# Kernel tuning notes

Hardware: AMD Instinct MI355X
Metric: run time of the kernel (lower is better)

Reference implementation:

```python
import jax, jax.numpy as jnp
import numpy as np

N_NODES = 50000
NEG_SLOPE = 0.2  # PyG GATConv default
EPS = 1e-16      # PyG softmax eps


def gat_conv(x, src, dst, W, a_s, a_d, b, n_nodes):
    """One PyG-style GATConv layer (concat heads). a_s/a_d: [H, C]."""
    H, C = a_s.shape
    h = (x @ W).reshape(n_nodes, H, C)                   # [N, H, C]
    al_s = jnp.sum(h * a_s[None], axis=-1)               # [N, H]
    al_d = jnp.sum(h * a_d[None], axis=-1)               # [N, H]
    e = jax.nn.leaky_relu(al_s[src] + al_d[dst], NEG_SLOPE)  # [E, H]
    # segment softmax over incoming edges of each destination node
    m = jax.ops.segment_max(e, dst, num_segments=n_nodes)
    m = jnp.where(jnp.isfinite(m), m, 0.0)
    ex = jnp.exp(e - m[dst])
    denom = jax.ops.segment_sum(ex, dst, num_segments=n_nodes)
    alpha = ex / (denom[dst] + EPS)                       # [E, H]
    out = jax.ops.segment_sum(alpha[:, :, None] * h[src], dst, num_segments=n_nodes)
    return out.reshape(n_nodes, H * C) + b                # concat heads + bias


def setup_inputs() -> dict:
    key = jax.random.key(0)
    ks = jax.random.split(key, 16)
    s = 0.05
    return {
        "x": jax.random.normal(ks[0], (N_NODES, 256), jnp.float32),
        "edge_index": jax.random.randint(ks[1], (2, 800000), 0, N_NODES, jnp.int64),
        "W1": jax.random.normal(ks[2], (256, 256), jnp.float32) * s,
        "as1": jax.random.normal(ks[3], (4, 64), jnp.float32) * s,
        "ad1": jax.random.normal(ks[4], (4, 64), jnp.float32) * s,
        "b1": jnp.zeros((256,), jnp.float32),
        "W2": jax.random.normal(ks[5], (256, 256), jnp.float32) * s,
        "as2": jax.random.normal(ks[6], (4, 64), jnp.float32) * s,
        "ad2": jax.random.normal(ks[7], (4, 64), jnp.float32) * s,
        "b2": jnp.zeros((256,), jnp.float32),
        "W3": jax.random.normal(ks[8], (256, 128), jnp.float32) * s,
        "as3": jax.random.normal(ks[9], (1, 128), jnp.float32) * s,
        "ad3": jax.random.normal(ks[10], (1, 128), jnp.float32) * s,
        "b3": jnp.zeros((128,), jnp.float32),
    }


def reference(x, edge_index, W1, as1, ad1, b1, W2, as2, ad2, b2, W3, as3, ad3, b3):
    n = x.shape[0]
    loop = jnp.arange(n, dtype=edge_index.dtype)
    src = jnp.concatenate([edge_index[0], loop])  # add_self_loops=True (PyG default)
    dst = jnp.concatenate([edge_index[1], loop])
    # F.dropout(p=0.6, training=False) -> identity in eval
    h = gat_conv(x, src, dst, W1, as1, ad1, b1, n)
    h = jax.nn.elu(h)  # gnn_act='elu'
    h = gat_conv(h, src, dst, W2, as2, ad2, b2, n)
    h = jax.nn.elu(h)
    h = gat_conv(h, src, dst, W3, as3, ad3, b3, n)
    return h
```

## Files before the change

### kernel.cpp

```cpp
#include <hip/hip_runtime.h>
#include <math.h>


#define NEG_SLOPE 0.2f
#define EPS_SM 1e-16f

typedef _Float16 half8 __attribute__((ext_vector_type(8)));
typedef _Float16 half4v __attribute__((ext_vector_type(4)));
typedef _Float16 half2v __attribute__((ext_vector_type(2)));
typedef float f32x4 __attribute__((ext_vector_type(4)));

__device__ __forceinline__ float wave_allred_sum(float v) {
#pragma unroll
    for (int o = 32; o > 0; o >>= 1) v += __shfl_xor(v, o, 64);
    return v;
}
__device__ __forceinline__ float4 lrelu4(float4 v) {
    v.x = (v.x < 0.f) ? NEG_SLOPE * v.x : v.x;
    v.y = (v.y < 0.f) ? NEG_SLOPE * v.y : v.y;
    v.z = (v.z < 0.f) ? NEG_SLOPE * v.z : v.z;
    v.w = (v.w < 0.f) ? NEG_SLOPE * v.w : v.w;
    return v;
}

__global__ void hist_kernel(const int* __restrict__ ei, int E, int N,
                            int* __restrict__ cnt) {
    int e = blockIdx.x * 256 + threadIdx.x;
    int ET = E + N;
    if (e >= ET) return;
    int dst = (e < E) ? ei[E + e] : (e - E);
    atomicAdd(&cnt[dst], 1);
}

__global__ void scan_block(const int* __restrict__ cnt, int n_cnt,
                           int* __restrict__ offs, int n_off,
                           int* __restrict__ bsums) {
    __shared__ int buf[1024];
    int gid = blockIdx.x * 1024 + threadIdx.x;
    int v = (gid < n_cnt) ? cnt[gid] : 0;
    buf[threadIdx.x] = v;
    __syncthreads();
#pragma unroll
    for (int off = 1; off < 1024; off <<= 1) {
        int t = (threadIdx.x >= off) ? buf[threadIdx.x - off] : 0;
        __syncthreads();
        buf[threadIdx.x] += t;
        __syncthreads();
    }
    if (gid < n_off) offs[gid] = buf[threadIdx.x] - v;
    if (threadIdx.x == 1023) bsums[blockIdx.x] = buf[1023];
}

__global__ void scan_sums(int* __restrict__ bsums, int nb) {
    int l = threadIdx.x;
    int v = (l < nb) ? bsums[l] : 0;
    int s = v;
#pragma unroll
    for (int o = 1; o < 64; o <<= 1) {
        int t = __shfl_up(s, o, 64);
        if (l >= o) s += t;
    }
    if (l < nb) bsums[l] = s - v;
}

__global__ void scan_add(int* __restrict__ offs, int n_off,
                         const int* __restrict__ bsums) {
    int gid = blockIdx.x * 1024 + threadIdx.x;
    if (gid < n_off) offs[gid] += bsums[blockIdx.x];
}

__global__ void fill_csr(const int* __restrict__ ei, int E, int N,
                         const int* __restrict__ offs, int* __restrict__ fil,
                         int* __restrict__ csr) {
    int e = blockIdx.x * 256 + threadIdx.x;
    int ET = E + N;
    if (e >= ET) return;
    int src, dst;
    if (e < E) { src = ei[e]; dst = ei[E + e]; }
    else       { src = dst = e - E; }
    int pos = offs[dst] + atomicAdd(&fil[dst], 1);
    csr[pos] = src;
}

__global__ void wcast_all(const float* __restrict__ W1,
                          const float* __restrict__ W2,
                          const float* __restrict__ W3,
                          _Float16* __restrict__ o1,
                          _Float16* __restrict__ o2,
                          _Float16* __restrict__ o3) {
    int i = blockIdx.x * 256 + threadIdx.x;
    const float* W; _Float16* o; int K = 256, N, s;
    if (i < 65536)        { W = W1; o = o1; N = 256; s = i; }
    else if (i < 131072)  { W = W2; o = o2; N = 256; s = i - 65536; }
    else if (i < 163840)  { W = W3; o = o3; N = 128; s = i - 131072; }
    else return;
    int n = s / K, k = s - n * K;
    o[s] = (_Float16)W[(size_t)k * N + n];
}

template <bool AF32>
__global__ __launch_bounds__(256) void gemm_wide64(
    const void* __restrict__ Ain, const _Float16* __restrict__ Bt,
    _Float16* __restrict__ C,
    const float* __restrict__ a_s, const float* __restrict__ a_d,
    float* __restrict__ als, float* __restrict__ ald, int M) {
    const int K = 256, N = 256;
    __shared__ _Float16 As[2][64][40], Bs[2][256][40];
    const int bm = blockIdx.x * 64;
    const int tid = threadIdx.x;
    const int w = tid >> 6, lane = tid & 63;
    const int wn = w * 64;
    const int l16 = lane & 15, q = lane >> 4;
    const int kq = q * 8;
    const int arow = tid >> 2, ak = (tid & 3) * 8;
    const int brow = tid;
    const int agrow = bm + arow;
    const int NT = K >> 5;

    f32x4 acc[4][4];
#pragma unroll
    for (int i = 0; i < 4; ++i)
#pragma unroll
        for (int j = 0; j < 4; ++j) acc[i][j] = (f32x4){0.f, 0.f, 0.f, 0.f};

    half8 ra, rb0, rb1, rb2, rb3;
    auto LOAD = [&](int kt) {
        if constexpr (AF32) {
            const float* Af = (const float*)Ain;
            float4 v0, v1;
            if (agrow < M) {
                const float4* ap = (const float4*)(Af + (size_t)agrow * K + kt + ak);
                v0 = ap[0]; v1 = ap[1];
            } else {
                v0 = v1 = make_float4(0.f, 0.f, 0.f, 0.f);
            }
            ra[0] = (_Float16)v0.x; ra[1] = (_Float16)v0.y;
            ra[2] = (_Float16)v0.z; ra[3] = (_Float16)v0.w;
            ra[4] = (_Float16)v1.x; ra[5] = (_Float16)v1.y;
            ra[6] = (_Float16)v1.z; ra[7] = (_Float16)v1.w;
        } else {
            const _Float16* Ah = (const _Float16*)Ain;
            if (agrow < M) {
                ra = *(const half8*)(Ah + (size_t)agrow * K + kt + ak);
            } else {
                ra = (half8)(_Float16)0;
            }
        }
        const half8* bp = (const half8*)(Bt + (size_t)brow * K + kt);
        rb0 = bp[0]; rb1 = bp[1]; rb2 = bp[2]; rb3 = bp[3];
    };
    auto STORE = [&](int nb) {
        *(half8*)&As[nb][arow][ak]  = ra;
        *(half8*)&Bs[nb][brow][0]   = rb0;
        *(half8*)&Bs[nb][brow][8]   = rb1;
        *(half8*)&Bs[nb][brow][16]  = rb2;
        *(half8*)&Bs[nb][brow][24]  = rb3;
    };

    LOAD(0);
    STORE(0);
    int cur = 0;
    for (int kb = 0; kb < NT; ++kb) {
        const bool more = (kb + 1) < NT;
        if (more) LOAD((kb + 1) * 32);
        __syncthreads();
        half8 a[4], b[4];
#pragma unroll
        for (int t = 0; t < 4; ++t) {
            a[t] = *(const half8*)&As[cur][t * 16 + l16][kq];
            b[t] = *(const half8*)&Bs[cur][wn + t * 16 + l16][kq];
        }
#pragma unroll
        for (int i = 0; i < 4; ++i)
#pragma unroll
            for (int j = 0; j < 4; ++j)
                acc[i][j] = __builtin_amdgcn_mfma_f32_16x16x32_f16(
                    a[i], b[j], acc[i][j], 0, 0, 0);
        if (more) STORE(cur ^ 1);
        cur ^= 1;
    }

#pragma unroll
    for (int i = 0; i < 4; ++i) {
#pragma unroll
        for (int r = 0; r < 4; ++r) {
            int orow = bm + i * 16 + q * 4 + r;
            float c0 = acc[i][0][r], c1 = acc[i][1][r];
            float c2 = acc[i][2][r], c3 = acc[i][3][r];
            if (orow < M) {
                _Float16* cp = C + (size_t)orow * N + wn + l16;
                cp[0]  = (_Float16)c0;
                cp[16] = (_Float16)c1;
                cp[32] = (_Float16)c2;
                cp[48] = (_Float16)c3;
            }
            {
                const int cg = wn + l16;
                float ps = c0 * a_s[cg] + c1 * a_s[cg + 16] +
                           c2 * a_s[cg + 32] + c3 * a_s[cg + 48];
                float pd = c0 * a_d[cg] + c1 * a_d[cg + 16] +
                           c2 * a_d[cg + 32] + c3 * a_d[cg + 48];
#pragma unroll
                for (int o = 1; o < 16; o <<= 1) {
                    ps += __shfl_xor(ps, o, 64);
                    pd += __shfl_xor(pd, o, 64);
                }
                if (l16 == 0 && orow < M) {
                    als[orow * 4 + w] = ps;
                    ald[orow * 4 + w] = pd;
                }
            }
        }
    }
}

__global__ __launch_bounds__(256) void gemm_f16_l3(
    const _Float16* __restrict__ Ain, const _Float16* __restrict__ Bt,
    _Float16* __restrict__ C,
    const float* __restrict__ a_s, const float* __restrict__ a_d,
    float* __restrict__ als, float* __restrict__ ald,
    int M, int N, int K) {
    __shared__ _Float16 As[2][128][40], Bs[2][128][40];
    __shared__ float s_als[128], s_ald[128];
    const int bm = blockIdx.y * 128;
    const int tid = threadIdx.x;
    const int w = tid >> 6, lane = tid & 63;
    const int wm = (w >> 1) * 64, wn = (w & 1) * 64;
    const int l16 = lane & 15, q = lane >> 4;
    const int kq = q * 8;
    const int sr = tid >> 1;
    const int sk = (tid & 1) * 16;
    const int row = bm + sr;
    const int NT = K >> 5;

    f32x4 acc[4][4];
#pragma unroll
    for (int i = 0; i < 4; ++i)
#pragma unroll
        for (int j = 0; j < 4; ++j) acc[i][j] = (f32x4){0.f, 0.f, 0.f, 0.f};

    half8 ra0, ra1, rb0, rb1;
    auto LOAD = [&](int kt) {
        if (row < M) {
            const half8* ap = (const half8*)(Ain + (size_t)row * K + kt + sk);
            ra0 = ap[0]; ra1 = ap[1];
        } else {
            ra0 = (half8)(_Float16)0; ra1 = (half8)(_Float16)0;
        }
        const half8* bp = (const half8*)(Bt + (size_t)sr * K + kt + sk);
        rb0 = bp[0]; rb1 = bp[1];
    };
    auto STORE = [&](int nb) {
        *(half8*)&As[nb][sr][sk]     = ra0;
        *(half8*)&As[nb][sr][sk + 8] = ra1;
        *(half8*)&Bs[nb][sr][sk]     = rb0;
        *(half8*)&Bs[nb][sr][sk + 8] = rb1;
    };

    LOAD(0);
    STORE(0);
    int cur = 0;
    for (int kb = 0; kb < NT; ++kb) {
        const bool more = (kb + 1) < NT;
        if (more) LOAD((kb + 1) * 32);
        __syncthreads();
        half8 a[4], b[4];
#pragma unroll
        for (int t = 0; t < 4; ++t) {
            a[t] = *(const half8*)&As[cur][wm + t * 16 + l16][kq];
            b[t] = *(const half8*)&Bs[cur][wn + t * 16 + l16][kq];
        }
#pragma unroll
        for (int i = 0; i < 4; ++i)
#pragma unroll
            for (int j = 0; j < 4; ++j)
                acc[i][j] = __builtin_amdgcn_mfma_f32_16x16x32_f16(
                    a[i], b[j], acc[i][j], 0, 0, 0);
        if (more) STORE(cur ^ 1);
        cur ^= 1;
    }

    __syncthreads();
    if (tid < 128) { s_als[tid] = 0.f; s_ald[tid] = 0.f; }
    __syncthreads();
#pragma unroll
    for (int i = 0; i < 4; ++i) {
#pragma unroll
        for (int r = 0; r < 4; ++r) {
            int orow = bm + wm + i * 16 + q * 4 + r;
            float c0 = acc[i][0][r], c1 = acc[i][1][r];
            float c2 = acc[i][2][r], c3 = acc[i][3][r];
            if (orow < M) {
                _Float16* cp = C + (size_t)orow * N + wn + l16;
                cp[0]  = (_Float16)c0;
                cp[16] = (_Float16)c1;
                cp[32] = (_Float16)c2;
                cp[48] = (_Float16)c3;
            }
            {
                const int cg = wn + l16;
                float ps = c0 * a_s[cg] + c1 * a_s[cg + 16] +
                           c2 * a_s[cg + 32] + c3 * a_s[cg + 48];
                float pd = c0 * a_d[cg] + c1 * a_d[cg + 16] +
                           c2 * a_d[cg + 32] + c3 * a_d[cg + 48];
#pragma unroll
                for (int o = 1; o < 16; o <<= 1) {
                    ps += __shfl_xor(ps, o, 64);
                    pd += __shfl_xor(pd, o, 64);
                }
                if (l16 == 0) {
                    atomicAdd(&s_als[wm + i * 16 + q * 4 + r], ps);
                    atomicAdd(&s_ald[wm + i * 16 + q * 4 + r], pd);
                }
            }
        }
    }
    __syncthreads();
    if (tid < 128) {
        int orow = bm + tid;
        if (orow < M) { als[orow] = s_als[tid]; ald[orow] = s_ald[tid]; }
    }
}

template <bool ACT>
__global__ __launch_bounds__(256) void aggregate_h4_f16(
    const _Float16* __restrict__ h, const float4* __restrict__ als4,
    const float4* __restrict__ ald4, const int* __restrict__ offs,
    const int* __restrict__ csr, const float* __restrict__ bias,
    _Float16* __restrict__ out, int Nn) {
    const int tid = threadIdx.x;
    const int w = tid >> 6;
    const int l = tid & 63;
    const int n = blockIdx.x * 4 + w;
    __shared__ float s_alpha[4][64][4];
    __shared__ int s_src[4][64];
    if (n >= Nn) return;

    const int base = offs[n];
    const int deg = offs[n + 1] - base;
    const float4 adv = ald4[n];
    const int head = l >> 4;

    float4 acc = make_float4(0.f, 0.f, 0.f, 0.f);
    float4 den = make_float4(0.f, 0.f, 0.f, 0.f);
    for (int c0 = 0; c0 < deg; c0 += 64) {
        const int cl = min(64, deg - c0);
        if (l < cl) {
            int s = csr[base + c0 + l];
            float4 a = als4[s];
            float4 sc = lrelu4(make_float4(a.x + adv.x, a.y + adv.y,
                                           a.z + adv.z, a.w + adv.w));
            float4 ex = make_float4(__expf(sc.x), __expf(sc.y),
                                    __expf(sc.z), __expf(sc.w));
            *(float4*)&s_alpha[w][l][0] = ex;
            s_src[w][l] = s;
            den.x += ex.x; den.y += ex.y; den.z += ex.z; den.w += ex.w;
        }
        int e = 0;
        for (; e + 4 <= cl; e += 4) {
            int s0 = s_src[w][e + 0], s1 = s_src[w][e + 1];
            int s2 = s_src[w][e + 2], s3 = s_src[w][e + 3];
            float a0 = s_alpha[w][e + 0][head];
            float a1 = s_alpha[w][e + 1][head];
            float a2 = s_alpha[w][e + 2][head];
            float a3 = s_alpha[w][e + 3][head];
            half4v hv0 = *(const half4v*)(h + (size_t)s0 * 256 + l * 4);
            half4v hv1 = *(const half4v*)(h + (size_t)s1 * 256 + l * 4);
            half4v hv2 = *(const half4v*)(h + (size_t)s2 * 256 + l * 4);
            half4v hv3 = *(const half4v*)(h + (size_t)s3 * 256 + l * 4);
            acc.x = fmaf(a0, (float)hv0[0], acc.x);
            acc.y = fmaf(a0, (float)hv0[1], acc.y);
            acc.z = fmaf(a0, (float)hv0[2], acc.z);
            acc.w = fmaf(a0, (float)hv0[3], acc.w);
            acc.x = fmaf(a1, (float)hv1[0], acc.x);
            acc.y = fmaf(a1, (float)hv1[1], acc.y);
            acc.z = fmaf(a1, (float)hv1[2], acc.z);
            acc.w = fmaf(a1, (float)hv1[3], acc.w);
            acc.x = fmaf(a2, (float)hv2[0], acc.x);
            acc.y = fmaf(a2, (float)hv2[1], acc.y);
            acc.z = fmaf(a2, (float)hv2[2], acc.z);
            acc.w = fmaf(a2, (float)hv2[3], acc.w);
            acc.x = fmaf(a3, (float)hv3[0], acc.x);
            acc.y = fmaf(a3, (float)hv3[1], acc.y);
            acc.z = fmaf(a3, (float)hv3[2], acc.z);
            acc.w = fmaf(a3, (float)hv3[3], acc.w);
        }
        for (; e < cl; ++e) {
            int s0 = s_src[w][e];
            float a0 = s_alpha[w][e][head];
            half4v hv0 = *(const half4v*)(h + (size_t)s0 * 256 + l * 4);
            acc.x = fmaf(a0, (float)hv0[0], acc.x);
            acc.y = fmaf(a0, (float)hv0[1], acc.y);
            acc.z = fmaf(a0, (float)hv0[2], acc.z);
            acc.w = fmaf(a0, (float)hv0[3], acc.w);
        }
    }
    den.x = wave_allred_sum(den.x); den.y = wave_allred_sum(den.y);
    den.z = wave_allred_sum(den.z); den.w = wave_allred_sum(den.w);
    float d = (head == 0) ? den.x : (head == 1) ? den.y
             : (head == 2) ? den.z : den.w;
    const float rc = 1.f / (d + EPS_SM);

    float4 bv = *(const float4*)(bias + l * 4);
    float4 r = make_float4(acc.x * rc + bv.x, acc.y * rc + bv.y,
                           acc.z * rc + bv.z, acc.w * rc + bv.w);
    if (ACT) {
        r.x = (r.x > 0.f) ? r.x : expm1f(r.x);
        r.y = (r.y > 0.f) ? r.y : expm1f(r.y);
        r.z = (r.z > 0.f) ? r.z : expm1f(r.z);
        r.w = (r.w > 0.f) ? r.w : expm1f(r.w);
    }
    half4v ov = {(_Float16)r.x, (_Float16)r.y, (_Float16)r.z, (_Float16)r.w};
    *(half4v*)(out + (size_t)n * 256 + l * 4) = ov;
}

__global__ __launch_bounds__(256) void aggregate_h1_f16(
    const _Float16* __restrict__ h, const float* __restrict__ als,
    const float* __restrict__ ald, const int* __restrict__ offs,
    const int* __restrict__ csr, const float* __restrict__ bias,
    float* __restrict__ out, int Nn) {
    const int tid = threadIdx.x;
    const int w = tid >> 6;
    const int l = tid & 63;
    const int n = blockIdx.x * 4 + w;
    __shared__ float s_alpha[4][64];
    __shared__ int s_src[4][64];
    if (n >= Nn) return;

    const int base = offs[n];
    const int deg = offs[n + 1] - base;
    const float ad_n = ald[n];

    float2 acc = make_float2(0.f, 0.f);
    float den = 0.f;
    for (int c0 = 0; c0 < deg; c0 += 64) {
        const int cl = min(64, deg - c0);
        if (l < cl) {
            int s = csr[base + c0 + l];
            float sc = als[s] + ad_n;
            sc = (sc < 0.f) ? NEG_SLOPE * sc : sc;
            float ex = __expf(sc);
            s_alpha[w][l] = ex;
            s_src[w][l] = s;
            den += ex;
        }
        int e = 0;
        for (; e + 4 <= cl; e += 4) {
            int s0 = s_src[w][e + 0], s1 = s_src[w][e + 1];
            int s2 = s_src[w][e + 2], s3 = s_src[w][e + 3];
            float a0 = s_alpha[w][e + 0], a1 = s_alpha[w][e + 1];
            float a2 = s_alpha[w][e + 2], a3 = s_alpha[w][e + 3];
            half2v v0 = *(const half2v*)(h + (size_t)s0 * 128 + l * 2);
            half2v v1 = *(const half2v*)(h + (size_t)s1 * 128 + l * 2);
            half2v v2 = *(const half2v*)(h + (size_t)s2 * 128 + l * 2);
            half2v v3 = *(const half2v*)(h + (size_t)s3 * 128 + l * 2);
            acc.x = fmaf(a0, (float)v0[0], acc.x); acc.y = fmaf(a0, (float)v0[1], acc.y);
            acc.x = fmaf(a1, (float)v1[0], acc.x); acc.y = fmaf(a1, (float)v1[1], acc.y);
            acc.x = fmaf(a2, (float)v2[0], acc.x); acc.y = fmaf(a2, (float)v2[1], acc.y);
            acc.x = fmaf(a3, (float)v3[0], acc.x); acc.y = fmaf(a3, (float)v3[1], acc.y);
        }
        for (; e < cl; ++e) {
            int s0 = s_src[w][e];
            float a0 = s_alpha[w][e];
            half2v v0 = *(const half2v*)(h + (size_t)s0 * 128 + l * 2);
            acc.x = fmaf(a0, (float)v0[0], acc.x); acc.y = fmaf(a0, (float)v0[1], acc.y);
        }
    }
    den = wave_allred_sum(den);
    const float rc = 1.f / (den + EPS_SM);
    float2 r = make_float2(acc.x * rc + bias[l * 2],
                           acc.y * rc + bias[l * 2 + 1]);
    *(float2*)(out + (size_t)n * 128 + l * 2) = r;
}

extern "C" void kernel_launch(void* const* d_in, const int* in_sizes, int n_in,
                              void* d_out, int out_size, void* d_ws,
                              size_t ws_size, hipStream_t stream) {
    const float* x   = (const float*)d_in[0];
    const int*   ei  = (const int*)d_in[1];
    const float* W1  = (const float*)d_in[2];
    const float* as1 = (const float*)d_in[3];
    const float* ad1 = (const float*)d_in[4];
    const float* b1  = (const float*)d_in[5];
    const float* W2  = (const float*)d_in[6];
    const float* as2 = (const float*)d_in[7];
    const float* ad2 = (const float*)d_in[8];
    const float* b2  = (const float*)d_in[9];
    const float* W3  = (const float*)d_in[10];
    const float* as3 = (const float*)d_in[11];
    const float* ad3 = (const float*)d_in[12];
    const float* b3  = (const float*)d_in[13];

    const int Nn = in_sizes[0] / 256;
    const int E  = in_sizes[1] / 2;
    const int ET = E + Nn;

    char* p = (char*)d_ws;
    _Float16* bufA = (_Float16*)p; p += (size_t)Nn * 256 * 2;
    _Float16* bufB = (_Float16*)p; p += (size_t)Nn * 256 * 2;
    float* als  = (float*)p; p += (size_t)Nn * 4 * 4;
    float* ald  = (float*)p; p += (size_t)Nn * 4 * 4;
    int* cnt  = (int*)p; p += (size_t)Nn * 4;
    int* fil  = (int*)p; p += (size_t)Nn * 4;
    int* offs = (int*)p; p += (size_t)(Nn + 1) * 4;
    int* bsums = (int*)p; p += 256 * 4;
    int* csr  = (int*)p; p += (size_t)ET * 4;
    p = (char*)(((uintptr_t)p + 15) & ~(uintptr_t)15);
    _Float16* wt1 = (_Float16*)p; p += 256 * 256 * 2;
    _Float16* wt2 = (_Float16*)p; p += 256 * 256 * 2;
    _Float16* wt3 = (_Float16*)p; p += 128 * 256 * 2;

    hipMemsetAsync(cnt, 0, (size_t)2 * Nn * sizeof(int), stream);
    int nbE = (ET + 255) / 256;
    hist_kernel<<<nbE, 256, 0, stream>>>(ei, E, Nn, cnt);
    wcast_all<<<(163840 + 255) / 256, 256, 0, stream>>>(W1, W2, W3, wt1, wt2, wt3);
    int nbS = (Nn + 1 + 1023) / 1024;
    scan_block<<<nbS, 1024, 0, stream>>>(cnt, Nn, offs, Nn + 1, bsums);
    scan_sums<<<1, 64, 0, stream>>>(bsums, nbS);
    scan_add<<<nbS, 1024, 0, stream>>>(offs, Nn + 1, bsums);
    fill_csr<<<nbE, 256, 0, stream>>>(ei, E, Nn, offs, fil, csr);

    const int gm64 = (Nn + 63) / 64;
    const int gm   = (Nn + 127) / 128;
    const int ga   = (Nn + 3) / 4;

    gemm_wide64<true><<<gm64, 256, 0, stream>>>(
        x, wt1, bufB, as1, ad1, als, ald, Nn);
    aggregate_h4_f16<true><<<ga, 256, 0, stream>>>(
        bufB, (const float4*)als, (const float4*)ald, offs, csr, b1, bufA, Nn);

    gemm_wide64<false><<<gm64, 256, 0, stream>>>(
        bufA, wt2, bufB, as2, ad2, als, ald, Nn);
    aggregate_h4_f16<true><<<ga, 256, 0, stream>>>(
        bufB, (const float4*)als, (const float4*)ald, offs, csr, b2, bufA, Nn);

    gemm_f16_l3<<<dim3(1, gm), 256, 0, stream>>>(
        bufA, wt3, bufB, as3, ad3, als, ald, Nn, 128, 256);
    aggregate_h1_f16<<<ga, 256, 0, stream>>>(
        bufB, als, ald, offs, csr, b3, (float*)d_out, Nn);
}
```

Baseline: 442.5 us.

## Fold attention vectors into weight matrix as extra GEMM columns; merge scan kernels

```diff
diff --git a/kernel.cpp b/kernel.cpp
--- a/kernel.cpp
+++ b/kernel.cpp
@@ -51,22 +51,18 @@
     if (threadIdx.x == 1023) bsums[blockIdx.x] = buf[1023];
 }
 
-__global__ void scan_sums(int* __restrict__ bsums, int nb) {
-    int l = threadIdx.x;
-    int v = (l < nb) ? bsums[l] : 0;
-    int s = v;
-#pragma unroll
-    for (int o = 1; o < 64; o <<= 1) {
-        int t = __shfl_up(s, o, 64);
-        if (l >= o) s += t;
-    }
-    if (l < nb) bsums[l] = s - v;
-}
-
 __global__ void scan_add(int* __restrict__ offs, int n_off,
                          const int* __restrict__ bsums) {
+    __shared__ int s_pref;
+    if (threadIdx.x < 64) {
+        int v = ((int)threadIdx.x < (int)blockIdx.x) ? bsums[threadIdx.x] : 0;
+#pragma unroll
+        for (int o = 32; o > 0; o >>= 1) v += __shfl_xor(v, o, 64);
+        if (threadIdx.x == 0) s_pref = v;
+    }
+    __syncthreads();
     int gid = blockIdx.x * 1024 + threadIdx.x;
-    if (gid < n_off) offs[gid] += bsums[blockIdx.x];
+    if (gid < n_off) offs[gid] += s_pref;
 }
 
 __global__ void fill_csr(const int* __restrict__ ei, int E, int N,
@@ -85,27 +81,61 @@
 __global__ void wcast_all(const float* __restrict__ W1,
                           const float* __restrict__ W2,
                           const float* __restrict__ W3,
+                          const float* __restrict__ as1, const float* __restrict__ ad1,
+                          const float* __restrict__ as2, const float* __restrict__ ad2,
+                          const float* __restrict__ as3, const float* __restrict__ ad3,
                           _Float16* __restrict__ o1,
                           _Float16* __restrict__ o2,
                           _Float16* __restrict__ o3) {
     int i = blockIdx.x * 256 + threadIdx.x;
-    const float* W; _Float16* o; int K = 256, N, s;
-    if (i < 65536)        { W = W1; o = o1; N = 256; s = i; }
-    else if (i < 131072)  { W = W2; o = o2; N = 256; s = i - 65536; }
-    else if (i < 163840)  { W = W3; o = o3; N = 128; s = i - 131072; }
-    else return;
-    int n = s / K, k = s - n * K;
-    o[s] = (_Float16)W[(size_t)k * N + n];
+    if (i < 65536) {
+        int n = i >> 8, k = i & 255;
+        o1[i] = (_Float16)W1[(size_t)k * 256 + n];
+    } else if (i < 131072) {
+        int s = i - 65536; int n = s >> 8, k = s & 255;
+        o2[s] = (_Float16)W2[(size_t)k * 256 + n];
+    } else if (i < 163840) {
+        int s = i - 131072; int n = s >> 8, k = s & 255;
+        o3[s] = (_Float16)W3[(size_t)k * 128 + n];
+    } else if (i < 163840 + 4096) {
+        int t = i - 163840; int j = t >> 8, k = t & 255;
+        float acc = 0.f;
+        if (j < 8) {
+            int h = j & 3;
+            const float* a = ((j < 4) ? as1 : ad1) + h * 64;
+            const float* wr = W1 + (size_t)k * 256 + h * 64;
+            for (int c = 0; c < 64; ++c) acc += wr[c] * a[c];
+        }
+        o1[65536 + t] = (_Float16)acc;
+    } else if (i < 163840 + 8192) {
+        int t = i - 163840 - 4096; int j = t >> 8, k = t & 255;
+        float acc = 0.f;
+        if (j < 8) {
+            int h = j & 3;
+            const float* a = ((j < 4) ? as2 : ad2) + h * 64;
+            const float* wr = W2 + (size_t)k * 256 + h * 64;
+            for (int c = 0; c < 64; ++c) acc += wr[c] * a[c];
+        }
+        o2[65536 + t] = (_Float16)acc;
+    } else if (i < 163840 + 12288) {
+        int t = i - 163840 - 8192; int j = t >> 8, k = t & 255;
+        float acc = 0.f;
+        if (j < 2) {
+            const float* a = (j == 0) ? as3 : ad3;
+            const float* wr = W3 + (size_t)k * 128;
+            for (int c = 0; c < 128; ++c) acc += wr[c] * a[c];
+        }
+        o3[32768 + t] = (_Float16)acc;
+    }
 }
 
 template <bool AF32>
 __global__ __launch_bounds__(256) void gemm_wide64(
     const void* __restrict__ Ain, const _Float16* __restrict__ Bt,
     _Float16* __restrict__ C,
-    const float* __restrict__ a_s, const float* __restrict__ a_d,
     float* __restrict__ als, float* __restrict__ ald, int M) {
     const int K = 256, N = 256;
-    __shared__ _Float16 As[2][64][40], Bs[2][256][40];
+    __shared__ _Float16 As[2][64][40], Bs[2][272][40];
     const int bm = blockIdx.x * 64;
     const int tid = threadIdx.x;
     const int w = tid >> 6, lane = tid & 63;
@@ -117,13 +147,15 @@
     const int agrow = bm + arow;
     const int NT = K >> 5;
 
-    f32x4 acc[4][4];
-#pragma unroll
-    for (int i = 0; i < 4; ++i)
+    f32x4 acc[4][4], acce[4];
+#pragma unroll
+    for (int i = 0; i < 4; ++i) {
 #pragma unroll
         for (int j = 0; j < 4; ++j) acc[i][j] = (f32x4){0.f, 0.f, 0.f, 0.f};
-
-    half8 ra, rb0, rb1, rb2, rb3;
+        acce[i] = (f32x4){0.f, 0.f, 0.f, 0.f};
+    }
+
+    half8 ra, rb0, rb1, rb2, rb3, rbe;
     auto LOAD = [&](int kt) {
         if constexpr (AF32) {
             const float* Af = (const float*)Ain;
@@ -148,6 +180,16 @@
         }
         const half8* bp = (const half8*)(Bt + (size_t)brow * K + kt);
         rb0 = bp[0]; rb1 = bp[1]; rb2 = bp[2]; rb3 = bp[3];
+        if (tid < 16) {
+            const half8* be = (const half8*)(Bt + (size_t)(256 + tid) * K + kt);
+            rbe = be[0];
+        }
+    };
+    auto LOADE = [&](int kt) {
+        if (tid < 64) {
+            int er = tid >> 2, ek = (tid & 3) * 8;
+            rbe = *(const half8*)(Bt + (size_t)(256 + er) * K + kt + ek);
+        }
     };
     auto STORE = [&](int nb) {
         *(half8*)&As[nb][arow][ak]  = ra;
@@ -155,14 +197,18 @@
         *(half8*)&Bs[nb][brow][8]   = rb1;
         *(half8*)&Bs[nb][brow][16]  = rb2;
         *(half8*)&Bs[nb][brow][24]  = rb3;
+        if (tid < 64) {
+            int er = tid >> 2, ek = (tid & 3) * 8;
+            *(half8*)&Bs[nb][256 + er][ek] = rbe;
+        }
     };
 
-    LOAD(0);
+    LOAD(0); LOADE(0);
     STORE(0);
     int cur = 0;
     for (int kb = 0; kb < NT; ++kb) {
         const bool more = (kb + 1) < NT;
-        if (more) LOAD((kb + 1) * 32);
+        if (more) { LOAD((kb + 1) * 32); LOADE((kb + 1) * 32); }
         __syncthreads();
         half8 a[4], b[4];
 #pragma unroll
@@ -176,6 +222,13 @@
             for (int j = 0; j < 4; ++j)
                 acc[i][j] = __builtin_amdgcn_mfma_f32_16x16x32_f16(
                     a[i], b[j], acc[i][j], 0, 0, 0);
+        if (w == 0) {
+            half8 be = *(const half8*)&Bs[cur][256 + l16][kq];
+#pragma unroll
+            for (int i = 0; i < 4; ++i)
+                acce[i] = __builtin_amdgcn_mfma_f32_16x16x32_f16(
+                    a[i], be, acce[i], 0, 0, 0);
+        }
         if (more) STORE(cur ^ 1);
         cur ^= 1;
     }
@@ -184,30 +237,26 @@
     for (int i = 0; i < 4; ++i) {
 #pragma unroll
         for (int r = 0; r < 4; ++r) {
-            int orow = bm + i * 16 + q * 4 + r;
-            float c0 = acc[i][0][r], c1 = acc[i][1][r];
-            float c2 = acc[i][2][r], c3 = acc[i][3][r];
+            int orow = bm + ((w == 0) ? 0 : 0) + i * 16 + q * 4 + r;
             if (orow < M) {
                 _Float16* cp = C + (size_t)orow * N + wn + l16;
-                cp[0]  = (_Float16)c0;
-                cp[16] = (_Float16)c1;
-                cp[32] = (_Float16)c2;
-                cp[48] = (_Float16)c3;
+                cp[0]  = (_Float16)acc[i][0][r];
+                cp[16] = (_Float16)acc[i][1][r];
+                cp[32] = (_Float16)acc[i][2][r];
+                cp[48] = (_Float16)acc[i][3][r];
             }
-            {
-                const int cg = wn + l16;
-                float ps = c0 * a_s[cg] + c1 * a_s[cg + 16] +
-                           c2 * a_s[cg + 32] + c3 * a_s[cg + 48];
-                float pd = c0 * a_d[cg] + c1 * a_d[cg + 16] +
-                           c2 * a_d[cg + 32] + c3 * a_d[cg + 48];
-#pragma unroll
-                for (int o = 1; o < 16; o <<= 1) {
-                    ps += __shfl_xor(ps, o, 64);
-                    pd += __shfl_xor(pd, o, 64);
-                }
-                if (l16 == 0 && orow < M) {
-                    als[orow * 4 + w] = ps;
-                    ald[orow * 4 + w] = pd;
+        }
+    }
+    if (w == 0) {
+#pragma unroll
+        for (int i = 0; i < 4; ++i) {
+#pragma unroll
+            for (int r = 0; r < 4; ++r) {
+                int orow = bm + i * 16 + q * 4 + r;
+                if (orow < M) {
+                    float c = acce[i][r];
+                    if (l16 < 4)      als[orow * 4 + l16] = c;
+                    else if (l16 < 8) ald[orow * 4 + (l16 - 4)] = c;
                 }
             }
         }
@@ -217,11 +266,9 @@
 __global__ __launch_bounds__(256) void gemm_f16_l3(
     const _Float16* __restrict__ Ain, const _Float16* __restrict__ Bt,
     _Float16* __restrict__ C,
-    const float* __restrict__ a_s, const float* __restrict__ a_d,
     float* __restrict__ als, float* __restrict__ ald,
     int M, int N, int K) {
-    __shared__ _Float16 As[2][128][40], Bs[2][128][40];
-    __shared__ float s_als[128], s_ald[128];
+    __shared__ _Float16 As[2][128][40], Bs[2][144][40];
     const int bm = blockIdx.y * 128;
     const int tid = threadIdx.x;
     const int w = tid >> 6, lane = tid & 63;
@@ -233,13 +280,15 @@
     const int row = bm + sr;
     const int NT = K >> 5;
 
-    f32x4 acc[4][4];
-#pragma unroll
-    for (int i = 0; i < 4; ++i)
+    f32x4 acc[4][4], acce[4];
+#pragma unroll
+    for (int i = 0; i < 4; ++i) {
 #pragma unroll
         for (int j = 0; j < 4; ++j) acc[i][j] = (f32x4){0.f, 0.f, 0.f, 0.f};
-
-    half8 ra0, ra1, rb0, rb1;
+        acce[i] = (f32x4){0.f, 0.f, 0.f, 0.f};
+    }
+
+    half8 ra0, ra1, rb0, rb1, rbe;
     auto LOAD = [&](int kt) {
         if (row < M) {
             const half8* ap = (const half8*)(Ain + (size_t)row * K + kt + sk);
@@ -249,12 +298,20 @@
         }
         const half8* bp = (const half8*)(Bt + (size_t)sr * K + kt + sk);
         rb0 = bp[0]; rb1 = bp[1];
+        if (tid < 64) {
+            int er = tid >> 2, ek = (tid & 3) * 8;
+            rbe = *(const half8*)(Bt + (size_t)(128 + er) * K + kt + ek);
+        }
     };
     auto STORE = [&](int nb) {
         *(half8*)&As[nb][sr][sk]     = ra0;
         *(half8*)&As[nb][sr][sk + 8] = ra1;
         *(half8*)&Bs[nb][sr][sk]     = rb0;
         *(half8*)&Bs[nb][sr][sk + 8] = rb1;
+        if (tid < 64) {
+            int er = tid >> 2, ek = (tid & 3) * 8;
+            *(half8*)&Bs[nb][128 + er][ek] = rbe;
+        }
     };
 
     LOAD(0);
@@ -276,49 +333,44 @@
             for (int j = 0; j < 4; ++j)
                 acc[i][j] = __builtin_amdgcn_mfma_f32_16x16x32_f16(
                     a[i], b[j], acc[i][j], 0, 0, 0);
+        if (wn == 0) {
+            half8 be = *(const half8*)&Bs[cur][128 + l16][kq];
+#pragma unroll
+            for (int i = 0; i < 4; ++i)
+                acce[i] = __builtin_amdgcn_mfma_f32_16x16x32_f16(
+                    a[i], be, acce[i], 0, 0, 0);
+        }
         if (more) STORE(cur ^ 1);
         cur ^= 1;
     }
 
-    __syncthreads();
-    if (tid < 128) { s_als[tid] = 0.f; s_ald[tid] = 0.f; }
-    __syncthreads();
 #pragma unroll
     for (int i = 0; i < 4; ++i) {
 #pragma unroll
         for (int r = 0; r < 4; ++r) {
             int orow = bm + wm + i * 16 + q * 4 + r;
-            float c0 = acc[i][0][r], c1 = acc[i][1][r];
-            float c2 = acc[i][2][r], c3 = acc[i][3][r];
             if (orow < M) {
                 _Float16* cp = C + (size_t)orow * N + wn + l16;
-                cp[0]  = (_Float16)c0;
-                cp[16] = (_Float16)c1;
-                cp[32] = (_Float16)c2;
-                cp[48] = (_Float16)c3;
+                cp[0]  = (_Float16)acc[i][0][r];
+                cp[16] = (_Float16)acc[i][1][r];
+                cp[32] = (_Float16)acc[i][2][r];
+                cp[48] = (_Float16)acc[i][3][r];
             }
-            {
-                const int cg = wn + l16;
-                float ps = c0 * a_s[cg] + c1 * a_s[cg + 16] +
-                           c2 * a_s[cg + 32] + c3 * a_s[cg + 48];
-                float pd = c0 * a_d[cg] + c1 * a_d[cg + 16] +
-                           c2 * a_d[cg + 32] + c3 * a_d[cg + 48];
-#pragma unroll
-                for (int o = 1; o < 16; o <<= 1) {
-                    ps += __shfl_xor(ps, o, 64);
-                    pd += __shfl_xor(pd, o, 64);
-                }
-                if (l16 == 0) {
-                    atomicAdd(&s_als[wm + i * 16 + q * 4 + r], ps);
-                    atomicAdd(&s_ald[wm + i * 16 + q * 4 + r], pd);
+        }
+    }
+    if (wn == 0) {
+#pragma unroll
+        for (int i = 0; i < 4; ++i) {
+#pragma unroll
+            for (int r = 0; r < 4; ++r) {
+                int orow = bm + wm + i * 16 + q * 4 + r;
+                if (orow < M) {
+                    float c = acce[i][r];
+                    if (l16 == 0)      als[orow] = c;
+                    else if (l16 == 1) ald[orow] = c;
                 }
             }
         }
-    }
-    __syncthreads();
-    if (tid < 128) {
-        int orow = bm + tid;
-        if (orow < M) { als[orow] = s_als[tid]; ald[orow] = s_ald[tid]; }
     }
 }
 
@@ -506,17 +558,17 @@
     int* bsums = (int*)p; p += 256 * 4;
     int* csr  = (int*)p; p += (size_t)ET * 4;
     p = (char*)(((uintptr_t)p + 15) & ~(uintptr_t)15);
-    _Float16* wt1 = (_Float16*)p; p += 256 * 256 * 2;
-    _Float16* wt2 = (_Float16*)p; p += 256 * 256 * 2;
-    _Float16* wt3 = (_Float16*)p; p += 128 * 256 * 2;
+    _Float16* wt1 = (_Float16*)p; p += 272 * 256 * 2;
+    _Float16* wt2 = (_Float16*)p; p += 272 * 256 * 2;
+    _Float16* wt3 = (_Float16*)p; p += 144 * 256 * 2;
 
     hipMemsetAsync(cnt, 0, (size_t)2 * Nn * sizeof(int), stream);
     int nbE = (ET + 255) / 256;
     hist_kernel<<<nbE, 256, 0, stream>>>(ei, E, Nn, cnt);
-    wcast_all<<<(163840 + 255) / 256, 256, 0, stream>>>(W1, W2, W3, wt1, wt2, wt3);
+    wcast_all<<<(163840 + 12288 + 255) / 256, 256, 0, stream>>>(
+        W1, W2, W3, as1, ad1, as2, ad2, as3, ad3, wt1, wt2, wt3);
     int nbS = (Nn + 1 + 1023) / 1024;
     scan_block<<<nbS, 1024, 0, stream>>>(cnt, Nn, offs, Nn + 1, bsums);
-    scan_sums<<<1, 64, 0, stream>>>(bsums, nbS);
     scan_add<<<nbS, 1024, 0, stream>>>(offs, Nn + 1, bsums);
     fill_csr<<<nbE, 256, 0, stream>>>(ei, E, Nn, offs, fil, csr);
 
@@ -525,17 +577,17 @@
     const int ga   = (Nn + 3) / 4;
 
     gemm_wide64<true><<<gm64, 256, 0, stream>>>(
-        x, wt1, bufB, as1, ad1, als, ald, Nn);
+        x, wt1, bufB, als, ald, Nn);
     aggregate_h4_f16<true><<<ga, 256, 0, stream>>>(
         bufB, (const float4*)als, (const float4*)ald, offs, csr, b1, bufA, Nn);
 
     gemm_wide64<false><<<gm64, 256, 0, stream>>>(
-        bufA, wt2, bufB, as2, ad2, als, ald, Nn);
+        bufA, wt2, bufB, als, ald, Nn);
     aggregate_h4_f16<true><<<ga, 256, 0, stream>>>(
         bufB, (const float4*)als, (const float4*)ald, offs, csr, b2, bufA, Nn);
 
     gemm_f16_l3<<<dim3(1, gm), 256, 0, stream>>>(
-        bufA, wt3, bufB, as3, ad3, als, ald, Nn, 128, 256);
+        bufA, wt3, bufB, als, ald, Nn, 128, 256);
     aggregate_h1_f16<<<ga, 256, 0, stream>>>(
         bufB, als, ald, offs, csr, b3, (float*)d_out, Nn);
 }
```

Result: no change. 437.2 us (-1.2%).
